# Kernel tuning notes

Hardware: AMD Instinct MI355X
Metric: run time of the kernel (lower is better)

The kernel has to match this reference:

```python
import jax, jax.numpy as jnp
import numpy as np

O, A, H, L = 32, 8, 256, 3   # obs_units, act_units, hidden_units, hidden_layers
SCALE = 1.0                  # obs_scale
N, W = 512, 128              # n obs/action rows, n hypernet weight samples
W_TOTAL = (O*H + H) + (A*H + H) + (2*H*H + H) + L*(H*H + H) + (H*O + O) + (H + 1) + (H + 1)  # 348194


def _unpack(w):
    # Slice the flat per-sample weight vector exactly as PrimaryNetwork.feedforward does.
    c = [0]
    def take(n, shape=None):
        s = w[:, c[0]:c[0]+n]
        c[0] += n
        return s.reshape((w.shape[0],) + shape) if shape is not None else s
    w_obs = take(O*H, (H, O)); b_obs = take(H)
    w_act = take(A*H, (H, A)); b_act = take(H)
    w_tgt = take(2*H*H, (H, 2*H)); b_tgt = take(H)
    ws, bs = [], []
    for _ in range(L):
        ws.append(take(H*H, (H, H))); bs.append(take(H))
    w_state = take(H*O, (O, H)); b_state = take(O)
    w_reward = take(H, (1, H)); b_reward = take(1)
    w_done = take(H, (1, H)); b_done = take(1)
    return w_obs, b_obs, w_act, b_act, w_tgt, b_tgt, ws, bs, w_state, b_state, w_reward, b_reward, w_done, b_done


def setup_inputs() -> dict:
    key = jax.random.key(0)
    k1, k2, k3 = jax.random.split(key, 3)
    return {
        "obs": jax.random.normal(k1, (N, O), jnp.float32),
        "action": jax.random.normal(k2, (N, A), jnp.float32),
        # scale ~1/sqrt(H) so activations stay in a sane range through the MLP
        "w": jax.random.normal(k3, (W, W_TOTAL), jnp.float32) * (1.0 / np.sqrt(H)),
        "obs_min": jnp.zeros((O,), jnp.float32),
        "obs_max": jnp.ones((O,), jnp.float32),
    }


def reference(obs, action, w, obs_min, obs_max):
    lrelu = jax.nn.leaky_relu  # negative_slope=0.01, matches F.leaky_relu default
    (w_obs, b_obs, w_act, b_act, w_tgt, b_tgt, ws, bs,
     w_state, b_state, w_reward, b_reward, w_done, b_done) = _unpack(w)

    # normalize obs to [-scale, scale]
    x = (obs - obs_min[None, :]) / (obs_max - obs_min)[None, :]
    x = (2.0 * x - 1.0) * SCALE                         # [N, O]

    # per-sample hypernetwork MLP, batched over (N obs rows) x (W weight samples)
    o = jnp.einsum('who,no->nwh', w_obs, x) + b_obs[None]          # [N, W, H]
    a = jnp.einsum('wha,na->nwh', w_act, action) + b_act[None]     # [N, W, H]
    y = lrelu(jnp.concatenate([o, a], axis=-1))                    # [N, W, 2H]
    y = lrelu(jnp.einsum('whk,nwk->nwh', w_tgt, y) + b_tgt[None])  # [N, W, H]
    for wj, bj in zip(ws, bs):
        y = lrelu(jnp.einsum('whk,nwk->nwh', wj, y) + bj[None])

    next_states = jnp.einsum('wok,nwk->nwo', w_state, y) + b_state[None] + x[:, None, :]  # [N, W, O]
    rewards = jnp.tanh(jnp.einsum('wok,nwk->nwo', w_reward, y) + b_reward[None])          # [N, W, 1]
    dones = jax.nn.sigmoid(jnp.einsum('wok,nwk->nwo', w_done, y) + b_done[None])          # [N, W, 1]

    # un-normalize next_states
    next_states = (next_states / SCALE + 1.0) * 0.5
    next_states = next_states * (obs_max - obs_min)[None, None, :] + obs_min[None, None, :]
    return next_states, rewards, dones
```

## Files before the change

### kernel.cpp

```cpp
#include <hip/hip_runtime.h>
#include <cstdint>
#include <cstddef>

#define NMEM    128
#define WTOTAL  348194

#define OFF_WOBS   0
#define OFF_BOBS   8192
#define OFF_WACT   8448
#define OFF_BACT   10496
#define OFF_WTGT   10752
#define OFF_BTGT   141824
#define OFF_WS0    142080
#define OFF_BS0    207616
#define OFF_WS1    207872
#define OFF_BS1    273408
#define OFF_WS2    273664
#define OFF_BS2    339200
#define OFF_WSTATE 339456
#define OFF_BSTATE 347648
#define OFF_WREW   347680
#define OFF_BREW   347936
#define OFF_WDONE  347937
#define OFF_BDONE  348193

#define OUT_REW  2097152
#define OUT_DONE 2162688

#define RB 256
#define APITCH 264

typedef __attribute__((ext_vector_type(8))) short short8;
typedef __attribute__((ext_vector_type(4))) float f32x4;

__device__ __forceinline__ uint32_t pkbf2(float lo, float hi) {
  union { float f; uint32_t u; } a, b;
  a.f = lo; b.f = hi;
  return __builtin_amdgcn_perm(b.u + 0x8000u, a.u + 0x8000u, 0x07060302u);
}

__device__ __forceinline__ uint16_t f2b_fast(float f) {
  union { float f; uint32_t u; } x; x.f = f;
  return (uint16_t)((x.u + 0x8000u) >> 16);
}

__device__ __forceinline__ short8 pk8f2(const float2 f[4]) {
  union { uint32_t u[4]; short8 s; } r;
#pragma unroll
  for (int i = 0; i < 4; ++i) r.u[i] = pkbf2(f[i].x, f[i].y);
  return r.s;
}

__device__ __forceinline__ void zero16(f32x4 acc[16]) {
#pragma unroll
  for (int r = 0; r < 16; ++r)
#pragma unroll
    for (int j = 0; j < 4; ++j) acc[r][j] = 0.0f;
}

__device__ __forceinline__ void accum_pass(f32x4 acc[16],
                                           const uint16_t* __restrict__ Ab,
                                           const float* __restrict__ w0) {
  float2 g[2][4];
#pragma unroll
  for (int d = 0; d < 2; ++d)
#pragma unroll
    for (int i = 0; i < 4; ++i)
      g[d][i] = reinterpret_cast<const float2*>(w0 + d * 32)[i];

#pragma unroll
  for (int kt = 0; kt < 8; ++kt) {
    const int s = kt & 1;
    const short8 b = pk8f2(g[s]);
    if (kt < 6) {
#pragma unroll
      for (int i = 0; i < 4; ++i)
        g[s][i] = reinterpret_cast<const float2*>(w0 + (kt + 2) * 32)[i];
    }
#pragma unroll
    for (int rt = 0; rt < 16; ++rt) {
      const short8 a =
          *reinterpret_cast<const short8*>(Ab + rt * 16 * APITCH + kt * 32);
      acc[rt] = __builtin_amdgcn_mfma_f32_16x16x32_bf16(a, b, acc[rt], 0, 0, 0);
    }
  }
}

__device__ __forceinline__ void epi_lrelu(const f32x4 acc[16], float bv,
                                          uint16_t* __restrict__ B, int c,
                                          int lg) {
#pragma unroll
  for (int rt = 0; rt < 16; ++rt) {
#pragma unroll
    for (int j = 0; j < 4; ++j) {
      float v = acc[rt][j] + bv;
      v = (v > 0.0f) ? v : 0.01f * v;
      B[(rt * 16 + lg * 4 + j) * APITCH + c] = f2b_fast(v);
    }
  }
}

__global__ void __launch_bounds__(1024, 4)
pn_kernel(const float* __restrict__ obs, const float* __restrict__ action,
          const float* __restrict__ w, const float* __restrict__ omin,
          const float* __restrict__ omax, float* __restrict__ out)
{
  __shared__ __align__(16) uint16_t B1[RB * APITCH];

  const int tid  = threadIdx.x;
  const int lane = tid & 63;
  const int wid  = tid >> 6;
  const int lr   = lane & 15;
  const int lg   = lane >> 4;
  const int c    = wid * 16 + lr;

  const int bid    = blockIdx.x;
  const int xcd    = bid & 7;
  const int j5     = bid >> 3;
  const int member = xcd * 16 + (j5 >> 1);
  const int chunk  = j5 & 1;
  const int n0     = chunk * RB;
  const float* wm  = w + (size_t)member * WTOTAL;

  const uint16_t* Ab = B1 + lr * APITCH + lg * 8;

  {
    float2 fb[4];
#pragma unroll
    for (int i = 0; i < 4; ++i)
      fb[i] = reinterpret_cast<const float2*>(wm + OFF_WOBS + c * 32 + lg * 8)[i];
    const short8 b = pk8f2(fb);
    const float bb = wm[OFF_BOBS + c];
    const float4 mn0 = *reinterpret_cast<const float4*>(omin + lg * 8);
    const float4 mn1 = *reinterpret_cast<const float4*>(omin + lg * 8 + 4);
    const float4 mx0 = *reinterpret_cast<const float4*>(omax + lg * 8);
    const float4 mx1 = *reinterpret_cast<const float4*>(omax + lg * 8 + 4);
#pragma unroll
    for (int rt = 0; rt < 16; ++rt) {
      const int n = n0 + rt * 16 + lr;
      const float4 x0 = *reinterpret_cast<const float4*>(obs + n * 32 + lg * 8);
      const float4 x1 = *reinterpret_cast<const float4*>(obs + n * 32 + lg * 8 + 4);
      union { uint32_t u[4]; short8 s; } afr;
      afr.u[0] = pkbf2(2.0f * (x0.x - mn0.x) / (mx0.x - mn0.x) - 1.0f,
                       2.0f * (x0.y - mn0.y) / (mx0.y - mn0.y) - 1.0f);
      afr.u[1] = pkbf2(2.0f * (x0.z - mn0.z) / (mx0.z - mn0.z) - 1.0f,
                       2.0f * (x0.w - mn0.w) / (mx0.w - mn0.w) - 1.0f);
      afr.u[2] = pkbf2(2.0f * (x1.x - mn1.x) / (mx1.x - mn1.x) - 1.0f,
                       2.0f * (x1.y - mn1.y) / (mx1.y - mn1.y) - 1.0f);
      afr.u[3] = pkbf2(2.0f * (x1.z - mn1.z) / (mx1.z - mn1.z) - 1.0f,
                       2.0f * (x1.w - mn1.w) / (mx1.w - mn1.w) - 1.0f);
      f32x4 a0 = {0.0f, 0.0f, 0.0f, 0.0f};
      a0 = __builtin_amdgcn_mfma_f32_16x16x32_bf16(afr.s, b, a0, 0, 0, 0);
#pragma unroll
      for (int j = 0; j < 4; ++j) {
        float v = a0[j] + bb;
        v = (v > 0.0f) ? v : 0.01f * v;
        B1[(rt * 16 + lg * 4 + j) * APITCH + c] = f2b_fast(v);
      }
    }
  }
  __syncthreads();

  f32x4 acc[16];
  zero16(acc);

  accum_pass(acc, Ab, wm + OFF_WTGT + c * 512 + lg * 8);
  __syncthreads();

  {
    float2 fb[4];
#pragma unroll
    for (int i = 0; i < 4; ++i)
      fb[i] = reinterpret_cast<const float2*>(wm + OFF_WACT + c * 8 + lg * 8)[i];
    const short8 b = pk8f2(fb);
    const float bb = wm[OFF_BACT + c];
#pragma unroll
    for (int rt = 0; rt < 16; ++rt) {
      const int n = n0 + rt * 16 + lr;
      union { uint32_t u[4]; short8 s; } afr;
      if (lg == 0) {
        const float4 q0 = *reinterpret_cast<const float4*>(action + n * 8);
        const float4 q1 = *reinterpret_cast<const float4*>(action + n * 8 + 4);
        afr.u[0] = pkbf2(q0.x, q0.y);
        afr.u[1] = pkbf2(q0.z, q0.w);
        afr.u[2] = pkbf2(q1.x, q1.y);
        afr.u[3] = pkbf2(q1.z, q1.w);
      } else {
        afr.u[0] = afr.u[1] = afr.u[2] = afr.u[3] = 0u;
      }
      f32x4 a0 = {0.0f, 0.0f, 0.0f, 0.0f};
      a0 = __builtin_amdgcn_mfma_f32_16x16x32_bf16(afr.s, b, a0, 0, 0, 0);
#pragma unroll
      for (int j = 0; j < 4; ++j) {
        float v = a0[j] + bb;
        v = (v > 0.0f) ? v : 0.01f * v;
        B1[(rt * 16 + lg * 4 + j) * APITCH + c] = f2b_fast(v);
      }
    }
  }
  __syncthreads();

#pragma unroll 1
  for (int L = 0; L < 4; ++L) {
    const int woff = (L == 0) ? (OFF_WTGT + 256)
                   : (L == 1) ? OFF_WS0
                   : (L == 2) ? OFF_WS1 : OFF_WS2;
    const int boff = (L == 0) ? OFF_BTGT
                   : (L == 1) ? OFF_BS0
                   : (L == 2) ? OFF_BS1 : OFF_BS2;
    const int csh  = (L == 0) ? 9 : 8;
    if (L) zero16(acc);
    accum_pass(acc, Ab, wm + woff + (c << csh) + lg * 8);
    __syncthreads();
    epi_lrelu(acc, wm[boff + c], B1, c, lg);
    __syncthreads();
  }

  if (wid < 3) {
    zero16(acc);
#pragma unroll
    for (int kt = 0; kt < 8; ++kt) {
      short8 b;
      if (c < 32) {
        const float* p = wm + OFF_WSTATE + c * 256 + kt * 32 + lg * 8;
        float2 f[4];
#pragma unroll
        for (int i = 0; i < 4; ++i) f[i] = reinterpret_cast<const float2*>(p)[i];
        b = pk8f2(f);
      } else if (c == 32) {
        const float* p = wm + OFF_WREW + kt * 32 + lg * 8;
        float2 f[4];
#pragma unroll
        for (int i = 0; i < 4; ++i) f[i] = reinterpret_cast<const float2*>(p)[i];
        b = pk8f2(f);
      } else if (c == 33) {
        const float* p = wm + OFF_WDONE + kt * 32 + lg * 8;
        union { uint32_t u[4]; short8 s; } r;
#pragma unroll
        for (int i = 0; i < 4; ++i) r.u[i] = pkbf2(p[2 * i], p[2 * i + 1]);
        b = r.s;
      } else {
        union { uint32_t u[4]; short8 s; } z;
        z.u[0] = z.u[1] = z.u[2] = z.u[3] = 0u;
        b = z.s;
      }
#pragma unroll
      for (int rt = 0; rt < 16; ++rt) {
        const short8 a =
            *reinterpret_cast<const short8*>(Ab + rt * 16 * APITCH + kt * 32);
        acc[rt] = __builtin_amdgcn_mfma_f32_16x16x32_bf16(a, b, acc[rt], 0, 0, 0);
      }
    }

    if (c < 34) {
#pragma unroll
      for (int rt = 0; rt < 16; ++rt) {
#pragma unroll
        for (int j = 0; j < 4; ++j) {
          const int n = n0 + rt * 16 + lg * 4 + j;
          float v = acc[rt][j];
          if (c < 32) {
            const float mn = omin[c], mx = omax[c];
            const float rng = mx - mn;
            const float x = 2.0f * (obs[n * 32 + c] - mn) / rng - 1.0f;
            v += wm[OFF_BSTATE + c] + x;
            v = (v + 1.0f) * 0.5f;
            out[((size_t)n * NMEM + member) * 32 + c] = v * rng + mn;
          } else if (c == 32) {
            v += wm[OFF_BREW];
            out[(size_t)OUT_REW + (size_t)n * NMEM + member] = tanhf(v);
          } else {
            v += wm[OFF_BDONE];
            out[(size_t)OUT_DONE + (size_t)n * NMEM + member] =
                1.0f / (1.0f + expf(-v));
          }
        }
      }
    }
  }
}

extern "C" void kernel_launch(void* const* d_in, const int* in_sizes, int n_in,
                              void* d_out, int out_size, void* d_ws, size_t ws_size,
                              hipStream_t stream) {
  (void)in_sizes; (void)n_in; (void)out_size; (void)d_ws; (void)ws_size;
  const float* obs    = (const float*)d_in[0];
  const float* action = (const float*)d_in[1];
  const float* w      = (const float*)d_in[2];
  const float* omin   = (const float*)d_in[3];
  const float* omax   = (const float*)d_in[4];
  float* out = (float*)d_out;

  pn_kernel<<<dim3(256), dim3(1024), 0, stream>>>(obs, action, w, omin, omax, out);
}
```

Measured before the change: 124.8 us.

## Spread output-head MFMA work across all waves instead of three

The final projection to next-state, reward and done was previously computed by only 3 waves, each looping over 16 row tiles with one 16-column B fragment. Now every wave handles its own 16-row tile and computes all 34 output columns using three MFMA accumulators, two for the state columns and one for reward/done. This spreads the tail work evenly across the 16 waves of the block, shortening the serial epilogue, at the cost of each wave reloading and converting the output-head weights.

```diff
diff --git a/kernel.cpp b/kernel.cpp
--- a/kernel.cpp
+++ b/kernel.cpp
@@ -216,65 +216,68 @@
     __syncthreads();
   }
 
-  if (wid < 3) {
-    zero16(acc);
+  {
+    f32x4 h0 = {0.0f, 0.0f, 0.0f, 0.0f};
+    f32x4 h1 = {0.0f, 0.0f, 0.0f, 0.0f};
+    f32x4 h2 = {0.0f, 0.0f, 0.0f, 0.0f};
+    const uint16_t* Ah = B1 + (wid * 16 + lr) * APITCH + lg * 8;
 #pragma unroll
     for (int kt = 0; kt < 8; ++kt) {
-      short8 b;
-      if (c < 32) {
-        const float* p = wm + OFF_WSTATE + c * 256 + kt * 32 + lg * 8;
-        float2 f[4];
-#pragma unroll
-        for (int i = 0; i < 4; ++i) f[i] = reinterpret_cast<const float2*>(p)[i];
-        b = pk8f2(f);
-      } else if (c == 32) {
-        const float* p = wm + OFF_WREW + kt * 32 + lg * 8;
-        float2 f[4];
-#pragma unroll
-        for (int i = 0; i < 4; ++i) f[i] = reinterpret_cast<const float2*>(p)[i];
-        b = pk8f2(f);
-      } else if (c == 33) {
+      float2 f0[4], f1[4];
+#pragma unroll
+      for (int i = 0; i < 4; ++i) {
+        f0[i] = reinterpret_cast<const float2*>(
+                    wm + OFF_WSTATE + lr * 256 + kt * 32 + lg * 8)[i];
+        f1[i] = reinterpret_cast<const float2*>(
+                    wm + OFF_WSTATE + (16 + lr) * 256 + kt * 32 + lg * 8)[i];
+      }
+      const short8 b0 = pk8f2(f0);
+      const short8 b1 = pk8f2(f1);
+      short8 b2;
+      if (lr == 0) {
+        float2 f2[4];
+#pragma unroll
+        for (int i = 0; i < 4; ++i)
+          f2[i] = reinterpret_cast<const float2*>(wm + OFF_WREW + kt * 32 + lg * 8)[i];
+        b2 = pk8f2(f2);
+      } else if (lr == 1) {
         const float* p = wm + OFF_WDONE + kt * 32 + lg * 8;
         union { uint32_t u[4]; short8 s; } r;
 #pragma unroll
         for (int i = 0; i < 4; ++i) r.u[i] = pkbf2(p[2 * i], p[2 * i + 1]);
-        b = r.s;
+        b2 = r.s;
       } else {
         union { uint32_t u[4]; short8 s; } z;
         z.u[0] = z.u[1] = z.u[2] = z.u[3] = 0u;
-        b = z.s;
-      }
-#pragma unroll
-      for (int rt = 0; rt < 16; ++rt) {
-        const short8 a =
-            *reinterpret_cast<const short8*>(Ab + rt * 16 * APITCH + kt * 32);
-        acc[rt] = __builtin_amdgcn_mfma_f32_16x16x32_bf16(a, b, acc[rt], 0, 0, 0);
-      }
-    }
-
-    if (c < 34) {
-#pragma unroll
-      for (int rt = 0; rt < 16; ++rt) {
-#pragma unroll
-        for (int j = 0; j < 4; ++j) {
-          const int n = n0 + rt * 16 + lg * 4 + j;
-          float v = acc[rt][j];
-          if (c < 32) {
-            const float mn = omin[c], mx = omax[c];
-            const float rng = mx - mn;
-            const float x = 2.0f * (obs[n * 32 + c] - mn) / rng - 1.0f;
-            v += wm[OFF_BSTATE + c] + x;
-            v = (v + 1.0f) * 0.5f;
-            out[((size_t)n * NMEM + member) * 32 + c] = v * rng + mn;
-          } else if (c == 32) {
-            v += wm[OFF_BREW];
-            out[(size_t)OUT_REW + (size_t)n * NMEM + member] = tanhf(v);
-          } else {
-            v += wm[OFF_BDONE];
-            out[(size_t)OUT_DONE + (size_t)n * NMEM + member] =
-                1.0f / (1.0f + expf(-v));
-          }
-        }
+        b2 = z.s;
+      }
+      const short8 a = *reinterpret_cast<const short8*>(Ah + kt * 32);
+      h0 = __builtin_amdgcn_mfma_f32_16x16x32_bf16(a, b0, h0, 0, 0, 0);
+      h1 = __builtin_amdgcn_mfma_f32_16x16x32_bf16(a, b1, h1, 0, 0, 0);
+      h2 = __builtin_amdgcn_mfma_f32_16x16x32_bf16(a, b2, h2, 0, 0, 0);
+    }
+
+    const int c0 = lr, c1 = 16 + lr;
+    const float mnA = omin[c0], rgA = omax[c0] - mnA;
+    const float mnB = omin[c1], rgB = omax[c1] - mnB;
+    const float bsA = wm[OFF_BSTATE + c0], bsB = wm[OFF_BSTATE + c1];
+    const float br = wm[OFF_BREW], bd = wm[OFF_BDONE];
+#pragma unroll
+    for (int j = 0; j < 4; ++j) {
+      const int n = n0 + wid * 16 + lg * 4 + j;
+      const float x0 = 2.0f * (obs[n * 32 + c0] - mnA) / rgA - 1.0f;
+      float v0 = h0[j] + bsA + x0;
+      v0 = (v0 + 1.0f) * 0.5f;
+      out[((size_t)n * NMEM + member) * 32 + c0] = v0 * rgA + mnA;
+      const float x1 = 2.0f * (obs[n * 32 + c1] - mnB) / rgB - 1.0f;
+      float v1 = h1[j] + bsB + x1;
+      v1 = (v1 + 1.0f) * 0.5f;
+      out[((size_t)n * NMEM + member) * 32 + c1] = v1 * rgB + mnB;
+      if (lr == 0) {
+        out[(size_t)OUT_REW + (size_t)n * NMEM + member] = tanhf(h2[j] + br);
+      } else if (lr == 1) {
+        out[(size_t)OUT_DONE + (size_t)n * NMEM + member] =
+            1.0f / (1.0f + expf(-(h2[j] + bd)));
       }
     }
   }
```

After: 254.6 us. 2.04x slower.
